# Performance work log

Hardware: AMD Instinct MI355X
Metric: run time of the kernel (lower is better)

Reference implementation:

```python
import jax, jax.numpy as jnp
import numpy as np

B, L, S, H, E, M = 16, 2048, 2048, 8, 64, 64  # batch, q len, kv len, heads, per-head dim, modes
SCALE = 1.0 / (512 * 512)  # 1/(in_channels*out_channels)


def setup_inputs() -> dict:
    key = jax.random.key(0)
    kq, kk, kv, kw1, kw2 = jax.random.split(key, 5)
    return {
        "q": jax.random.normal(kq, (B, L, H, E), dtype=jnp.float32),
        "k": jax.random.normal(kk, (B, S, H, E), dtype=jnp.float32),
        "v": jax.random.normal(kv, (B, S, H, E), dtype=jnp.float32),
        "weights_real": SCALE * jax.random.uniform(kw1, (H, E, E, M), dtype=jnp.float32),
        "weights_imag": SCALE * jax.random.uniform(kw2, (H, E, E, M), dtype=jnp.float32),
        "mask": jnp.zeros((1,), dtype=bool),  # unused by forward (kept for signature parity)
    }


def reference(q, k, v, weights_real, weights_imag, mask):
    # [B, L, H, E] -> [B, H, E, L]
    _q = jnp.transpose(q, (0, 2, 3, 1))
    _k = jnp.transpose(k, (0, 2, 3, 1))
    _v = jnp.transpose(v, (0, 2, 3, 1))

    # rFFT along time; mode_select_method='else' => index = range(M), a contiguous slice
    Qf = jnp.fft.rfft(_q, axis=-1)[..., :M]  # [B, H, E, M] complex
    Kf = jnp.fft.rfft(_k, axis=-1)[..., :M]
    Vf = jnp.fft.rfft(_v, axis=-1)[..., :M]

    # cross attention in frequency domain
    QK = jnp.einsum('bhex,bhey->bhxy', Qf, Kf)  # [B, H, M, M] complex
    QK = jnp.tanh(QK.real) + 1j * jnp.tanh(QK.imag)  # 'tanh' activation on re/im
    QKV = jnp.einsum('bhxy,bhey->bhex', QK, Vf)  # [B, H, E, M]

    W = (weights_real + 1j * weights_imag).astype(jnp.complex64)  # [H, E, O, M]
    QKVW = jnp.einsum('bhex,heox->bhox', QKV, W)  # [B, H, O, M]

    # scatter selected modes back into full half-spectrum, then inverse FFT
    Y = jnp.zeros((B, H, E, L // 2 + 1), dtype=jnp.complex64).at[..., :M].set(QKVW)
    y = jnp.fft.irfft(Y, n=L, axis=-1)  # [B, H, O, L] real
    return jnp.transpose(y, (0, 3, 1, 2))  # [B, L, H, O]
```

## Files before the change

### kernel.cpp

```cpp
#include <hip/hip_runtime.h>
#include <hip/hip_fp16.h>
#include <math.h>


#define NB 16
#define NL 2048
#define NH 8
#define NE 64
#define NM 64
#define NHE 512

typedef unsigned short ushort_t;
typedef __attribute__((ext_vector_type(8))) short short8;
typedef __attribute__((ext_vector_type(8))) _Float16 half8;
typedef __attribute__((ext_vector_type(4))) float f32x4;

__device__ inline void gld_lds16(const void* g, void* l) {
    __builtin_amdgcn_global_load_lds((const __attribute__((address_space(1))) unsigned int*)g,
                                     (__attribute__((address_space(3))) unsigned int*)l, 16, 0, 0);
}

__global__ __launch_bounds__(256) void k_tables_gemm(ushort_t* __restrict__ Twh,
                                                     ushort_t* __restrict__ Twl) {
    int i = blockIdx.x * 256 + threadIdx.x;
    int kj = i & 7;
    int l  = (i >> 3) & 63;
    int g  = (i >> 9) & 7;
    int ks = i >> 12;
    int mp = g * 16 + (l & 15);
    int kk = (l >> 4) * 8 + kj;
    int t = ks * 32 + kk;
    int m = mp >> 1;
    float ang = (float)((6.283185307179586476925287 / (double)NL) * (double)((m * t) & (NL - 1)));
    float val = (mp & 1) ? -sinf(ang) : cosf(ang);
    unsigned cb = __float_as_uint(val);
    ushort_t h = (ushort_t)(cb >> 16);
    float lo = val - __uint_as_float(cb & 0xffff0000u);
    unsigned lb = __float_as_uint(lo);
    unsigned r = lb + 0x7fffu + ((lb >> 16) & 1u);
    Twh[i] = h;
    Twl[i] = (ushort_t)(r >> 16);
}

__global__ __launch_bounds__(256) void k_tables_idft(ushort_t* __restrict__ Ih) {
    int i = blockIdx.x * 256 + threadIdx.x;
    int j = i & 7;
    int l = (i >> 3) & 63;
    int f = (i >> 9) & 15;
    int ks = (i >> 13) & 3;
    int tt = i >> 15;
    int t = tt * 256 + f * 16 + (l & 15);
    int kk = ks * 32 + (l >> 4) * 8 + j;
    int x = kk >> 1;
    float ang = (float)((6.283185307179586476925287 / (double)NL) * (double)((t * x) & (NL - 1)));
    float val = (kk & 1) ? -sinf(ang) : cosf(ang);
    Ih[i] = __half_as_ushort(__float2half(val));
}

__global__ __launch_bounds__(256, 3) void k_gemm(
    const float* __restrict__ q, const float* __restrict__ k, const float* __restrict__ v,
    const ushort_t* __restrict__ Twh, const ushort_t* __restrict__ Twl,
    float* __restrict__ Part) {
    const int bx = blockIdx.x & 7;
    const int kq = blockIdx.x >> 3;
    const int b  = blockIdx.y;
    const int z  = blockIdx.z;
    const float* __restrict__ in = (z == 0) ? q : ((z == 1) ? k : v);

    const int tid  = threadIdx.x;
    const int wid  = tid >> 6;
    const int lane = tid & 63;
    const int lr   = lane & 15;
    const int lg   = lane >> 4;
    const int wy   = wid >> 1;
    const int wx   = wid & 1;
    const int he0  = bx * 64;
    const int fx   = lg & 1;

    __shared__ float    As[2][32 * 64];
    __shared__ ushort_t Bh[2][4096];
    __shared__ ushort_t Bl[2][4096];

    f32x4 acc[2][4];
#pragma unroll
    for (int f = 0; f < 2; ++f)
#pragma unroll
        for (int j = 0; j < 4; ++j) acc[f][j] = (f32x4){0.f, 0.f, 0.f, 0.f};

    const size_t in_blk = ((size_t)b * NL + (size_t)kq * 1024) * NHE + he0;

#define STAGE(n, ksn)                                                                 \
    {                                                                                 \
        const ushort_t* gh = Twh + (size_t)(kq * 32 + (ksn)) * 4096;                  \
        const ushort_t* gl = Twl + (size_t)(kq * 32 + (ksn)) * 4096;                  \
        gld_lds16(gh + (size_t)tid * 8, &Bh[n][tid * 8]);                             \
        gld_lds16(gh + (size_t)(tid + 256) * 8, &Bh[n][(tid + 256) * 8]);             \
        gld_lds16(gl + (size_t)tid * 8, &Bl[n][tid * 8]);                             \
        gld_lds16(gl + (size_t)(tid + 256) * 8, &Bl[n][(tid + 256) * 8]);             \
        const float* ga = in + in_blk + (size_t)(ksn) * 32 * NHE;                     \
        _Pragma("unroll")                                                             \
        for (int p = 0; p < 2; ++p) {                                                 \
            int u = tid + p * 256;                                                    \
            int tloc = u >> 4, hc = u & 15;                                           \
            int hcs = hc ^ (((tloc >> 3) & 1) << 2);                                  \
            gld_lds16(ga + (size_t)tloc * NHE + hcs * 4, &As[n][u * 4]);              \
        }                                                                             \
    }

    STAGE(0, 0);

    int cur = 0;
    for (int ks = 0; ks < 32; ++ks) {
        __syncthreads();
        if (ks + 1 < 32) STAGE(cur ^ 1, ks + 1);

        const float* ac = &As[cur][0];
        const ushort_t* bhc = &Bh[cur][0];
        const ushort_t* blc = &Bl[cur][0];

        short8 bh8[4], bl8[4];
#pragma unroll
        for (int j = 0; j < 4; ++j) {
            bh8[j] = *(const short8*)&bhc[((wx * 4 + j) * 64 + lane) * 8];
            bl8[j] = *(const short8*)&blc[((wx * 4 + j) * 64 + lane) * 8];
        }

#pragma unroll
        for (int f = 0; f < 2; ++f) {
            const int col = wy * 32 + ((f ^ fx) << 4) + lr;
            float xa[8];
#pragma unroll
            for (int j = 0; j < 8; ++j) xa[j] = ac[(8 * lg + j) * 64 + col];
            union { unsigned u[4]; short8 s; } uh, ul;
#pragma unroll
            for (int p = 0; p < 4; ++p) {
                unsigned b0 = __float_as_uint(xa[2 * p]);
                unsigned b1 = __float_as_uint(xa[2 * p + 1]);
                uh.u[p] = (b0 >> 16) | (b1 & 0xffff0000u);
                float l0 = xa[2 * p]     - __uint_as_float(b0 & 0xffff0000u);
                float l1 = xa[2 * p + 1] - __uint_as_float(b1 & 0xffff0000u);
                unsigned lw;
                asm("v_cvt_pk_bf16_f32 %0, %1, %2" : "=v"(lw) : "v"(l0), "v"(l1));
                ul.u[p] = lw;
            }
#pragma unroll
            for (int j = 0; j < 4; ++j) {
                acc[f][j] = __builtin_amdgcn_mfma_f32_16x16x32_bf16(uh.s, bh8[j], acc[f][j], 0, 0, 0);
                acc[f][j] = __builtin_amdgcn_mfma_f32_16x16x32_bf16(ul.s, bh8[j], acc[f][j], 0, 0, 0);
                acc[f][j] = __builtin_amdgcn_mfma_f32_16x16x32_bf16(uh.s, bl8[j], acc[f][j], 0, 0, 0);
            }
        }
        cur ^= 1;
    }
#undef STAGE

    float* pout = Part + (size_t)(z * 2 + kq) * 1048576;
#pragma unroll
    for (int f = 0; f < 2; ++f) {
#pragma unroll
        for (int j = 0; j < 4; ++j) {
            const int col = wx * 64 + j * 16 + lr;
#pragma unroll
            for (int r = 0; r < 4; ++r) {
                const int he = he0 + wy * 32 + f * 16 + 4 * lg + r;
                pout[((size_t)b * NHE + he) * 128 + col] = acc[f][j][r];
            }
        }
    }
}

__global__ __launch_bounds__(256) void k_reduce(
    const float4* __restrict__ Part, float4* __restrict__ Qf,
    float4* __restrict__ Kf, float4* __restrict__ Vf) {
    int i = blockIdx.x * 256 + threadIdx.x;
    int z = i >> 18;
    int r = i & 262143;
    float4 a = Part[(size_t)(z * 2 + 0) * 262144 + r];
    float4 b = Part[(size_t)(z * 2 + 1) * 262144 + r];
    float4 s = make_float4(a.x + b.x, a.y + b.y, a.z + b.z, a.w + b.w);
    float4* o = (z == 0) ? Qf : ((z == 1) ? Kf : Vf);
    o[r] = s;
}

__global__ __launch_bounds__(256) void k_qk(
    const float2* __restrict__ Qf, const float2* __restrict__ Kf,
    float2* __restrict__ QKt) {
    const int bh = blockIdx.x;
    const int xh = blockIdx.y;
    const int tid = threadIdx.x;
    __shared__ float2 Qs[64 * 34];
    __shared__ float2 Ks[64 * 66];

    const float2* Qbase = Qf + (size_t)bh * (NE * NM);
    const float2* Kbase = Kf + (size_t)bh * (NE * NM);
#pragma unroll
    for (int j = 0; j < 4; ++j) {
        int n = tid + j * 256;
        int e = n >> 4, c = n & 15;
        float4 val = ((const float4*)(Qbase + e * NM + xh * 32))[c];
        *((float4*)&Qs[e * 34 + c * 2]) = val;
    }
#pragma unroll
    for (int j = 0; j < 8; ++j) {
        int n = tid + j * 256;
        int e = n >> 5, c = n & 31;
        float4 val = ((const float4*)(Kbase + e * NM))[c];
        *((float4*)&Ks[e * 66 + c * 2]) = val;
    }
    __syncthreads();

    const int yq = tid & 31, xq = tid >> 5;
    float accr[4][2], acci[4][2];
#pragma unroll
    for (int i = 0; i < 4; ++i)
#pragma unroll
        for (int j = 0; j < 2; ++j) { accr[i][j] = 0.f; acci[i][j] = 0.f; }

    for (int e = 0; e < 64; ++e) {
        float4 qa = *((float4*)&Qs[e * 34 + xq * 4]);
        float4 qb = *((float4*)&Qs[e * 34 + xq * 4 + 2]);
        float4 kk = *((float4*)&Ks[e * 66 + yq * 2]);
        float qr[4] = {qa.x, qa.z, qb.x, qb.z};
        float qi[4] = {qa.y, qa.w, qb.y, qb.w};
        float kr[2] = {kk.x, kk.z};
        float ki[2] = {kk.y, kk.w};
#pragma unroll
        for (int i = 0; i < 4; ++i) {
#pragma unroll
            for (int j = 0; j < 2; ++j) {
                accr[i][j] += qr[i] * kr[j] - qi[i] * ki[j];
                acci[i][j] += qr[i] * ki[j] + qi[i] * kr[j];
            }
        }
    }
    const int x0 = xh * 32 + xq * 4;
#pragma unroll
    for (int i = 0; i < 4; ++i) {
        float4 sv = make_float4(tanhf(accr[i][0]), tanhf(acci[i][0]),
                                tanhf(accr[i][1]), tanhf(acci[i][1]));
        *((float4*)&QKt[(size_t)bh * 4096 + (x0 + i) * 64 + yq * 2]) = sv;
    }
}

__global__ __launch_bounds__(256) void k_qkv(
    const float2* __restrict__ Vf, const float2* __restrict__ QKt,
    float2* __restrict__ QKV) {
    const int bh = blockIdx.x;
    const int eh = blockIdx.y;
    const int tid = threadIdx.x;
    __shared__ float2 Vs[32 * 66];
    __shared__ float2 Ps[64 * 66];

    const float2* Vbase = Vf + (size_t)bh * (NE * NM) + eh * 32 * NM;
    const float2* Pbase = QKt + (size_t)bh * 4096;
#pragma unroll
    for (int j = 0; j < 4; ++j) {
        int n = tid + j * 256;
        int r = n >> 5, c = n & 31;
        float4 val = ((const float4*)(Vbase + r * NM))[c];
        *((float4*)&Vs[r * 66 + c * 2]) = val;
    }
#pragma unroll
    for (int j = 0; j < 8; ++j) {
        int n = tid + j * 256;
        int r = n >> 5, c = n & 31;
        float4 val = ((const float4*)(Pbase + r * NM))[c];
        *((float4*)&Ps[r * 66 + c * 2]) = val;
    }
    __syncthreads();

    const int xq = tid & 15, eq2 = tid >> 4;
    const int x0 = xq * 4, e0 = eq2 * 2;
    float accr[2][4], acci[2][4];
#pragma unroll
    for (int i = 0; i < 2; ++i)
#pragma unroll
        for (int j = 0; j < 4; ++j) { accr[i][j] = 0.f; acci[i][j] = 0.f; }

    for (int yy = 0; yy < 64; ++yy) {
        float2 v0 = Vs[(e0 + 0) * 66 + yy];
        float2 v1 = Vs[(e0 + 1) * 66 + yy];
        float2 p0 = Ps[(x0 + 0) * 66 + yy];
        float2 p1 = Ps[(x0 + 1) * 66 + yy];
        float2 p2 = Ps[(x0 + 2) * 66 + yy];
        float2 p3 = Ps[(x0 + 3) * 66 + yy];
        float pr[4] = {p0.x, p1.x, p2.x, p3.x};
        float pi[4] = {p0.y, p1.y, p2.y, p3.y};
#pragma unroll
        for (int j = 0; j < 4; ++j) {
            accr[0][j] += v0.x * pr[j] - v0.y * pi[j];
            acci[0][j] += v0.x * pi[j] + v0.y * pr[j];
            accr[1][j] += v1.x * pr[j] - v1.y * pi[j];
            acci[1][j] += v1.x * pi[j] + v1.y * pr[j];
        }
    }
#pragma unroll
    for (int e = 0; e < 2; ++e) {
        float2* obase = QKV + (size_t)bh * 4096 + (eh * 32 + e0 + e) * 64 + x0;
        float4 s0 = make_float4(accr[e][0], acci[e][0], accr[e][1], acci[e][1]);
        float4 s1 = make_float4(accr[e][2], acci[e][2], accr[e][3], acci[e][3]);
        ((float4*)obase)[0] = s0;
        ((float4*)obase)[1] = s1;
    }
}

__global__ __launch_bounds__(256) void k_wt(
    const float* __restrict__ wr, const float* __restrict__ wi,
    float2* __restrict__ Wt) {
    const int e = blockIdx.x, h = blockIdx.y;
    const int tid = threadIdx.x;
    __shared__ float lr[64 * 68];
    __shared__ float li[64 * 68];
    const float* rbase = wr + (size_t)(h * NE + e) * NE * NM;
    const float* ibase = wi + (size_t)(h * NE + e) * NE * NM;
#pragma unroll
    for (int j = 0; j < 4; ++j) {
        int n = tid + j * 256;
        int o = n >> 4, x4 = n & 15;
        float4 r4 = ((const float4*)(rbase + o * NM))[x4];
        float4 i4 = ((const float4*)(ibase + o * NM))[x4];
        *((float4*)&lr[o * 68 + x4 * 4]) = r4;
        *((float4*)&li[o * 68 + x4 * 4]) = i4;
    }
    __syncthreads();
#pragma unroll
    for (int j = 0; j < 16; ++j) {
        int n = tid + j * 256;
        int x = n >> 6, o = n & 63;
        Wt[((size_t)(h * NM + x) * NE + e) * NE + o] =
            make_float2(lr[o * 68 + x], li[o * 68 + x]);
    }
}

__global__ __launch_bounds__(256) void k_qkvw(
    const float2* __restrict__ QKV, const float2* __restrict__ Wt,
    float2* __restrict__ QKVWs) {
    const int x = blockIdx.x, h = blockIdx.y;
    const int tid = threadIdx.x;
    const int o = tid & 63, bq = tid >> 6;
    float accr[4], acci[4];
#pragma unroll
    for (int j = 0; j < 4; ++j) { accr[j] = 0.f; acci[j] = 0.f; }

    const float2* wbase = Wt + (size_t)(h * NM + x) * NE * NE + o;
    for (int e = 0; e < 64; ++e) {
        float2 w = wbase[(size_t)e * NE];
#pragma unroll
        for (int j = 0; j < 4; ++j) {
            int b = bq * 4 + j;
            float2 a = QKV[((size_t)(b * NH + h) * NE + e) * NM + x];
            accr[j] += a.x * w.x - a.y * w.y;
            acci[j] += a.x * w.y + a.y * w.x;
        }
    }
    const float sc = (x == 0) ? 0.5f : 1.0f;
#pragma unroll
    for (int j = 0; j < 4; ++j) {
        int b = bq * 4 + j;
        QKVWs[((size_t)(b * NH + h) * NM + x) * NE + o] =
            make_float2(accr[j] * sc, acci[j] * sc);
    }
}

__global__ __launch_bounds__(256, 3) void k_idft(
    const float2* __restrict__ QKVWs, const ushort_t* __restrict__ Ih,
    float* __restrict__ yout) {
    const int tt = blockIdx.x;
    const int bh = blockIdx.y;
    const int b = bh >> 3, h = bh & 7;
    const int tid = threadIdx.x;
    const int wid = tid >> 6;
    const int lane = tid & 63;
    const int lr = lane & 15;
    const int lg = lane >> 4;

    __shared__ ushort_t Ta[8192];
    __shared__ unsigned Xs[4096];

    const float2* xb = QKVWs + (size_t)bh * 4096;
#pragma unroll
    for (int r = 0; r < 16; ++r) {
        int i = tid + r * 256;
        int x = i >> 6, o = i & 63;
        float2 val = xb[i];
        int ks = x >> 4;
        int lane2 = (((x & 15) >> 2) << 4) | (o & 15);
        int jn = o >> 4;
        unsigned pk = (unsigned)__half_as_ushort(__float2half(val.x)) |
                      ((unsigned)__half_as_ushort(__float2half(val.y)) << 16);
        Xs[((ks * 4 + jn) * 64 + lane2) * 4 + (x & 3)] = pk;
    }
    {
        const ushort_t* gh = Ih + (size_t)(tt * 4) * 8192;
#pragma unroll
        for (int p = 0; p < 4; ++p)
            gld_lds16(gh + (size_t)(tid + p * 256) * 8, &Ta[(tid + p * 256) * 8]);
    }
    __syncthreads();

    f32x4 acc[4][4];
#pragma unroll
    for (int m = 0; m < 4; ++m)
#pragma unroll
        for (int n = 0; n < 4; ++n) acc[m][n] = (f32x4){0.f, 0.f, 0.f, 0.f};

    const ushort_t* XsS = (const ushort_t*)Xs;
    for (int ks = 0; ks < 4; ++ks) {
        half8 ah[4], bx_[4];
#pragma unroll
        for (int m = 0; m < 4; ++m)
            ah[m] = *(const half8*)&Ta[((wid * 4 + m) * 64 + lane) * 8];
#pragma unroll
        for (int n = 0; n < 4; ++n)
            bx_[n] = *(const half8*)&XsS[((ks * 4 + n) * 64 + lane) * 8];
#pragma unroll
        for (int m = 0; m < 4; ++m)
#pragma unroll
            for (int n = 0; n < 4; ++n)
                acc[m][n] = __builtin_amdgcn_mfma_f32_16x16x32_f16(ah[m], bx_[n], acc[m][n], 0, 0, 0);
        if (ks < 3) {
            __syncthreads();
            const ushort_t* gh = Ih + (size_t)(tt * 4 + ks + 1) * 8192;
#pragma unroll
            for (int p = 0; p < 4; ++p)
                gld_lds16(gh + (size_t)(tid + p * 256) * 8, &Ta[(tid + p * 256) * 8]);
            __syncthreads();
        }
    }

    const int t0 = tt * 256 + wid * 64;
    const float inv = 1.f / 1024.f;
#pragma unroll
    for (int m = 0; m < 4; ++m) {
#pragma unroll
        for (int n = 0; n < 4; ++n) {
            const int o = n * 16 + lr;
#pragma unroll
            for (int r = 0; r < 4; ++r) {
                const int t = t0 + m * 16 + lg * 4 + r;
                yout[(((size_t)b * NL + t) * NH + h) * NE + o] = acc[m][n][r] * inv;
            }
        }
    }
}

extern "C" void kernel_launch(void* const* d_in, const int* in_sizes, int n_in,
                              void* d_out, int out_size, void* d_ws, size_t ws_size,
                              hipStream_t stream) {
    const float* q  = (const float*)d_in[0];
    const float* k  = (const float*)d_in[1];
    const float* v  = (const float*)d_in[2];
    const float* wr = (const float*)d_in[3];
    const float* wi = (const float*)d_in[4];
    float* out = (float*)d_out;

    char* w = (char*)d_ws;
    ushort_t* Twh  = (ushort_t*)w;
    ushort_t* Twl  = (ushort_t*)(w + 524288);
    ushort_t* Ih   = (ushort_t*)(w + 1048576);
    float2*   Qf   = (float2*)(w + 2097152);
    float2*   Kf   = (float2*)(w + 6291456);
    float2*   Vf   = (float2*)(w + 10485760);
    float*    Part = (float*)(w + 14680064);
    float2*   QKt  = (float2*)(w + 14680064);
    float2*   QKV  = (float2*)(w + 18874368);
    float2*   Wt   = (float2*)(w + 23068672);
    float2*   QKVWs= (float2*)(w + 39845888);

    hipLaunchKernelGGL(k_tables_gemm, dim3(1024), dim3(256), 0, stream, Twh, Twl);
    hipLaunchKernelGGL(k_tables_idft, dim3(1024), dim3(256), 0, stream, Ih);
    hipLaunchKernelGGL(k_gemm, dim3(16, 16, 3), dim3(256), 0, stream,
                       q, k, v, Twh, Twl, Part);
    hipLaunchKernelGGL(k_reduce, dim3(3072), dim3(256), 0, stream,
                       (const float4*)Part, (float4*)Qf, (float4*)Kf, (float4*)Vf);
    hipLaunchKernelGGL(k_qk, dim3(128, 2), dim3(256), 0, stream, Qf, Kf, QKt);
    hipLaunchKernelGGL(k_qkv, dim3(128, 2), dim3(256), 0, stream, Vf, QKt, QKV);
    hipLaunchKernelGGL(k_wt, dim3(64, 8), dim3(256), 0, stream, wr, wi, Wt);
    hipLaunchKernelGGL(k_qkvw, dim3(64, 8), dim3(256), 0, stream, QKV, Wt, QKVWs);
    hipLaunchKernelGGL(k_idft, dim3(8, 128), dim3(256), 0, stream, QKVWs, Ih, out);
}
```

Before: 155.3 us.

## Widen DFT GEMM tile to 128 channels and load A directly into registers

The forward-DFT GEMM kernel now has each block cover 128 head-channels instead of 64, with each wave owning 32 rows and all 128 frequency columns. The grid halves, so each twiddle tile staged in LDS is reused by twice as many rows. The fp32 input tile no longer goes through LDS; it is read straight from global memory into registers, double-buffered across an unrolled pair of k-steps, before the bf16 hi/lo split. This removes LDS traffic and LDS reads for A, but raises register pressure from 64 accumulator registers plus the prefetch buffers. It also gives fewer blocks (384) to fill the GPU and uses uncoalesced per-lane strided global loads.

```diff
diff --git a/kernel.cpp b/kernel.cpp
--- a/kernel.cpp
+++ b/kernel.cpp
@@ -61,8 +61,8 @@
     const float* __restrict__ q, const float* __restrict__ k, const float* __restrict__ v,
     const ushort_t* __restrict__ Twh, const ushort_t* __restrict__ Twl,
     float* __restrict__ Part) {
-    const int bx = blockIdx.x & 7;
-    const int kq = blockIdx.x >> 3;
+    const int bx = blockIdx.x & 3;
+    const int kq = blockIdx.x >> 2;
     const int b  = blockIdx.y;
     const int z  = blockIdx.z;
     const float* __restrict__ in = (z == 0) ? q : ((z == 1) ? k : v);
@@ -72,24 +72,21 @@
     const int lane = tid & 63;
     const int lr   = lane & 15;
     const int lg   = lane >> 4;
-    const int wy   = wid >> 1;
-    const int wx   = wid & 1;
-    const int he0  = bx * 64;
-    const int fx   = lg & 1;
-
-    __shared__ float    As[2][32 * 64];
+
     __shared__ ushort_t Bh[2][4096];
     __shared__ ushort_t Bl[2][4096];
 
-    f32x4 acc[2][4];
+    f32x4 acc[2][8];
 #pragma unroll
     for (int f = 0; f < 2; ++f)
 #pragma unroll
-        for (int j = 0; j < 4; ++j) acc[f][j] = (f32x4){0.f, 0.f, 0.f, 0.f};
-
-    const size_t in_blk = ((size_t)b * NL + (size_t)kq * 1024) * NHE + he0;
-
-#define STAGE(n, ksn)                                                                 \
+        for (int g = 0; g < 8; ++g) acc[f][g] = (f32x4){0.f, 0.f, 0.f, 0.f};
+
+    const float* pA = in + ((size_t)b * NL + (size_t)kq * 1024) * NHE + bx * 128 + wid * 32 + lr;
+
+    float arE[2][8], arO[2][8];
+
+#define STAGE_B(n, ksn)                                                               \
     {                                                                                 \
         const ushort_t* gh = Twh + (size_t)(kq * 32 + (ksn)) * 4096;                  \
         const ushort_t* gl = Twl + (size_t)(kq * 32 + (ksn)) * 4096;                  \
@@ -97,73 +94,81 @@
         gld_lds16(gh + (size_t)(tid + 256) * 8, &Bh[n][(tid + 256) * 8]);             \
         gld_lds16(gl + (size_t)tid * 8, &Bl[n][tid * 8]);                             \
         gld_lds16(gl + (size_t)(tid + 256) * 8, &Bl[n][(tid + 256) * 8]);             \
-        const float* ga = in + in_blk + (size_t)(ksn) * 32 * NHE;                     \
+    }
+
+#define LOADA(ar, ksn)                                                                \
+    {                                                                                 \
         _Pragma("unroll")                                                             \
-        for (int p = 0; p < 2; ++p) {                                                 \
-            int u = tid + p * 256;                                                    \
-            int tloc = u >> 4, hc = u & 15;                                           \
-            int hcs = hc ^ (((tloc >> 3) & 1) << 2);                                  \
-            gld_lds16(ga + (size_t)tloc * NHE + hcs * 4, &As[n][u * 4]);              \
+        for (int f = 0; f < 2; ++f) {                                                 \
+            _Pragma("unroll")                                                         \
+            for (int j = 0; j < 8; ++j)                                               \
+                ar[f][j] = pA[(size_t)((ksn) * 32 + lg * 8 + j) * NHE + f * 16];      \
         }                                                                             \
     }
 
-    STAGE(0, 0);
-
-    int cur = 0;
-    for (int ks = 0; ks < 32; ++ks) {
+#define COMPUTE(ar, n)                                                                \
+    {                                                                                 \
+        short8 ah[2], al[2];                                                          \
+        _Pragma("unroll")                                                             \
+        for (int f = 0; f < 2; ++f) {                                                 \
+            union { unsigned u[4]; short8 s; } uh, ul;                                \
+            _Pragma("unroll")                                                         \
+            for (int p = 0; p < 4; ++p) {                                             \
+                unsigned b0 = __float_as_uint(ar[f][2 * p]);                          \
+                unsigned b1 = __float_as_uint(ar[f][2 * p + 1]);                      \
+                uh.u[p] = (b0 >> 16) | (b1 & 0xffff0000u);                            \
+                float l0 = ar[f][2 * p]     - __uint_as_float(b0 & 0xffff0000u);      \
+                float l1 = ar[f][2 * p + 1] - __uint_as_float(b1 & 0xffff0000u);      \
+                unsigned lw;                                                          \
+                asm("v_cvt_pk_bf16_f32 %0, %1, %2" : "=v"(lw) : "v"(l0), "v"(l1));    \
+                ul.u[p] = lw;                                                         \
+            }                                                                         \
+            ah[f] = uh.s; al[f] = ul.s;                                               \
+        }                                                                             \
+        _Pragma("unroll")                                                             \
+        for (int g = 0; g < 8; ++g) {                                                 \
+            short8 bh8 = *(const short8*)&Bh[n][(g * 64 + lane) * 8];                 \
+            short8 bl8 = *(const short8*)&Bl[n][(g * 64 + lane) * 8];                 \
+            _Pragma("unroll")                                                         \
+            for (int f = 0; f < 2; ++f) {                                             \
+                acc[f][g] = __builtin_amdgcn_mfma_f32_16x16x32_bf16(ah[f], bh8, acc[f][g], 0, 0, 0); \
+                acc[f][g] = __builtin_amdgcn_mfma_f32_16x16x32_bf16(al[f], bh8, acc[f][g], 0, 0, 0); \
+                acc[f][g] = __builtin_amdgcn_mfma_f32_16x16x32_bf16(ah[f], bl8, acc[f][g], 0, 0, 0); \
+            }                                                                         \
+        }                                                                             \
+    }
+
+    STAGE_B(0, 0);
+    LOADA(arE, 0);
+
+#pragma unroll 1
+    for (int k2 = 0; k2 < 16; ++k2) {
+        const int ksB = 2 * k2 + 1;
         __syncthreads();
-        if (ks + 1 < 32) STAGE(cur ^ 1, ks + 1);
-
-        const float* ac = &As[cur][0];
-        const ushort_t* bhc = &Bh[cur][0];
-        const ushort_t* blc = &Bl[cur][0];
-
-        short8 bh8[4], bl8[4];
-#pragma unroll
-        for (int j = 0; j < 4; ++j) {
-            bh8[j] = *(const short8*)&bhc[((wx * 4 + j) * 64 + lane) * 8];
-            bl8[j] = *(const short8*)&blc[((wx * 4 + j) * 64 + lane) * 8];
-        }
-
-#pragma unroll
-        for (int f = 0; f < 2; ++f) {
-            const int col = wy * 32 + ((f ^ fx) << 4) + lr;
-            float xa[8];
-#pragma unroll
-            for (int j = 0; j < 8; ++j) xa[j] = ac[(8 * lg + j) * 64 + col];
-            union { unsigned u[4]; short8 s; } uh, ul;
-#pragma unroll
-            for (int p = 0; p < 4; ++p) {
-                unsigned b0 = __float_as_uint(xa[2 * p]);
-                unsigned b1 = __float_as_uint(xa[2 * p + 1]);
-                uh.u[p] = (b0 >> 16) | (b1 & 0xffff0000u);
-                float l0 = xa[2 * p]     - __uint_as_float(b0 & 0xffff0000u);
-                float l1 = xa[2 * p + 1] - __uint_as_float(b1 & 0xffff0000u);
-                unsigned lw;
-                asm("v_cvt_pk_bf16_f32 %0, %1, %2" : "=v"(lw) : "v"(l0), "v"(l1));
-                ul.u[p] = lw;
-            }
-#pragma unroll
-            for (int j = 0; j < 4; ++j) {
-                acc[f][j] = __builtin_amdgcn_mfma_f32_16x16x32_bf16(uh.s, bh8[j], acc[f][j], 0, 0, 0);
-                acc[f][j] = __builtin_amdgcn_mfma_f32_16x16x32_bf16(ul.s, bh8[j], acc[f][j], 0, 0, 0);
-                acc[f][j] = __builtin_amdgcn_mfma_f32_16x16x32_bf16(uh.s, bl8[j], acc[f][j], 0, 0, 0);
-            }
-        }
-        cur ^= 1;
-    }
-#undef STAGE
+        STAGE_B(1, ksB);
+        LOADA(arO, ksB);
+        COMPUTE(arE, 0);
+        __syncthreads();
+        if (k2 < 15) {
+            STAGE_B(0, ksB + 1);
+            LOADA(arE, ksB + 1);
+        }
+        COMPUTE(arO, 1);
+    }
+#undef STAGE_B
+#undef LOADA
+#undef COMPUTE
 
     float* pout = Part + (size_t)(z * 2 + kq) * 1048576;
 #pragma unroll
     for (int f = 0; f < 2; ++f) {
 #pragma unroll
-        for (int j = 0; j < 4; ++j) {
-            const int col = wx * 64 + j * 16 + lr;
+        for (int g = 0; g < 8; ++g) {
+            const int col = g * 16 + lr;
 #pragma unroll
             for (int r = 0; r < 4; ++r) {
-                const int he = he0 + wy * 32 + f * 16 + 4 * lg + r;
-                pout[((size_t)b * NHE + he) * 128 + col] = acc[f][j][r];
+                const int he = bx * 128 + wid * 32 + f * 16 + 4 * lg + r;
+                pout[((size_t)b * NHE + he) * 128 + col] = acc[f][g][r];
             }
         }
     }
@@ -469,7 +474,7 @@
 
     hipLaunchKernelGGL(k_tables_gemm, dim3(1024), dim3(256), 0, stream, Twh, Twl);
     hipLaunchKernelGGL(k_tables_idft, dim3(1024), dim3(256), 0, stream, Ih);
-    hipLaunchKernelGGL(k_gemm, dim3(16, 16, 3), dim3(256), 0, stream,
+    hipLaunchKernelGGL(k_gemm, dim3(8, 16, 3), dim3(256), 0, stream,
                        q, k, v, Twh, Twl, Part);
     hipLaunchKernelGGL(k_reduce, dim3(3072), dim3(256), 0, stream,
                        (const float4*)Part, (float4*)Qf, (float4*)Kf, (float4*)Vf);
```

Result: faster. 150.9 us (-2.8%).

## Fuse split-K reduction, QK tanh, and QKV into one kernel; merge table kernels

Applied to the files above, without the earlier changes.

Replaces the separate reduce, QK and QKV kernels with one kernel. It sums the two split-K partials directly while loading into LDS, computes tanh(QK) for half of the x modes, keeps it in shared memory, then loads V and produces QKV for that half. The two twiddle-table kernels are merged into one launch. This removes the intermediate Qf/Kf/Vf and QKt global round trips and cuts four launches, in exchange for each block redundantly re-reducing the K and V partials.

```diff
diff --git a/kernel.cpp b/kernel.cpp
--- a/kernel.cpp
+++ b/kernel.cpp
@@ -20,41 +20,43 @@
                                      (__attribute__((address_space(3))) unsigned int*)l, 16, 0, 0);
 }
 
-__global__ __launch_bounds__(256) void k_tables_gemm(ushort_t* __restrict__ Twh,
-                                                     ushort_t* __restrict__ Twl) {
-    int i = blockIdx.x * 256 + threadIdx.x;
-    int kj = i & 7;
-    int l  = (i >> 3) & 63;
-    int g  = (i >> 9) & 7;
-    int ks = i >> 12;
-    int mp = g * 16 + (l & 15);
-    int kk = (l >> 4) * 8 + kj;
-    int t = ks * 32 + kk;
-    int m = mp >> 1;
-    float ang = (float)((6.283185307179586476925287 / (double)NL) * (double)((m * t) & (NL - 1)));
-    float val = (mp & 1) ? -sinf(ang) : cosf(ang);
-    unsigned cb = __float_as_uint(val);
-    ushort_t h = (ushort_t)(cb >> 16);
-    float lo = val - __uint_as_float(cb & 0xffff0000u);
-    unsigned lb = __float_as_uint(lo);
-    unsigned r = lb + 0x7fffu + ((lb >> 16) & 1u);
-    Twh[i] = h;
-    Twl[i] = (ushort_t)(r >> 16);
-}
-
-__global__ __launch_bounds__(256) void k_tables_idft(ushort_t* __restrict__ Ih) {
-    int i = blockIdx.x * 256 + threadIdx.x;
-    int j = i & 7;
-    int l = (i >> 3) & 63;
-    int f = (i >> 9) & 15;
-    int ks = (i >> 13) & 3;
-    int tt = i >> 15;
-    int t = tt * 256 + f * 16 + (l & 15);
-    int kk = ks * 32 + (l >> 4) * 8 + j;
-    int x = kk >> 1;
-    float ang = (float)((6.283185307179586476925287 / (double)NL) * (double)((t * x) & (NL - 1)));
-    float val = (kk & 1) ? -sinf(ang) : cosf(ang);
-    Ih[i] = __half_as_ushort(__float2half(val));
+__global__ __launch_bounds__(256) void k_tables(ushort_t* __restrict__ Twh,
+                                                ushort_t* __restrict__ Twl,
+                                                ushort_t* __restrict__ Ih) {
+    const int blk = blockIdx.x;
+    if (blk < 1024) {
+        int i = blk * 256 + threadIdx.x;
+        int kj = i & 7;
+        int l  = (i >> 3) & 63;
+        int g  = (i >> 9) & 7;
+        int ks = i >> 12;
+        int mp = g * 16 + (l & 15);
+        int kk = (l >> 4) * 8 + kj;
+        int t = ks * 32 + kk;
+        int m = mp >> 1;
+        float ang = (float)((6.283185307179586476925287 / (double)NL) * (double)((m * t) & (NL - 1)));
+        float val = (mp & 1) ? -sinf(ang) : cosf(ang);
+        unsigned cb = __float_as_uint(val);
+        ushort_t h = (ushort_t)(cb >> 16);
+        float lo = val - __uint_as_float(cb & 0xffff0000u);
+        unsigned lb = __float_as_uint(lo);
+        unsigned r = lb + 0x7fffu + ((lb >> 16) & 1u);
+        Twh[i] = h;
+        Twl[i] = (ushort_t)(r >> 16);
+    } else {
+        int i = (blk - 1024) * 256 + threadIdx.x;
+        int j = i & 7;
+        int l = (i >> 3) & 63;
+        int f = (i >> 9) & 15;
+        int ks = (i >> 13) & 3;
+        int tt = i >> 15;
+        int t = tt * 256 + f * 16 + (l & 15);
+        int kk = ks * 32 + (l >> 4) * 8 + j;
+        int x = kk >> 1;
+        float ang = (float)((6.283185307179586476925287 / (double)NL) * (double)((t * x) & (NL - 1)));
+        float val = (kk & 1) ? -sinf(ang) : cosf(ang);
+        Ih[i] = __half_as_ushort(__float2half(val));
+    }
 }
 
 __global__ __launch_bounds__(256, 3) void k_gemm(
@@ -169,43 +171,40 @@
     }
 }
 
-__global__ __launch_bounds__(256) void k_reduce(
-    const float4* __restrict__ Part, float4* __restrict__ Qf,
-    float4* __restrict__ Kf, float4* __restrict__ Vf) {
-    int i = blockIdx.x * 256 + threadIdx.x;
-    int z = i >> 18;
-    int r = i & 262143;
-    float4 a = Part[(size_t)(z * 2 + 0) * 262144 + r];
-    float4 b = Part[(size_t)(z * 2 + 1) * 262144 + r];
-    float4 s = make_float4(a.x + b.x, a.y + b.y, a.z + b.z, a.w + b.w);
-    float4* o = (z == 0) ? Qf : ((z == 1) ? Kf : Vf);
-    o[r] = s;
-}
-
-__global__ __launch_bounds__(256) void k_qk(
-    const float2* __restrict__ Qf, const float2* __restrict__ Kf,
-    float2* __restrict__ QKt) {
+__global__ __launch_bounds__(256) void k_qkqkv(
+    const float* __restrict__ Part, float2* __restrict__ QKV) {
     const int bh = blockIdx.x;
     const int xh = blockIdx.y;
     const int tid = threadIdx.x;
-    __shared__ float2 Qs[64 * 34];
-    __shared__ float2 Ks[64 * 66];
-
-    const float2* Qbase = Qf + (size_t)bh * (NE * NM);
-    const float2* Kbase = Kf + (size_t)bh * (NE * NM);
+
+    __shared__ float2 bufA[64 * 34];
+    __shared__ float2 bufB[64 * 66];
+
+    const float4* P0 = (const float4*)Part;
+    const float4* P1 = P0 + 262144;
+    const float4* P2 = P0 + 2 * 262144;
+    const float4* P3 = P0 + 3 * 262144;
+    const float4* P4 = P0 + 4 * 262144;
+    const float4* P5 = P0 + 5 * 262144;
+    const size_t fb = (size_t)bh * 2048;
+
 #pragma unroll
     for (int j = 0; j < 4; ++j) {
         int n = tid + j * 256;
         int e = n >> 4, c = n & 15;
-        float4 val = ((const float4*)(Qbase + e * NM + xh * 32))[c];
-        *((float4*)&Qs[e * 34 + c * 2]) = val;
+        float4 a = P0[fb + e * 32 + xh * 16 + c];
+        float4 b = P1[fb + e * 32 + xh * 16 + c];
+        *((float4*)&bufA[e * 34 + c * 2]) =
+            make_float4(a.x + b.x, a.y + b.y, a.z + b.z, a.w + b.w);
     }
 #pragma unroll
     for (int j = 0; j < 8; ++j) {
         int n = tid + j * 256;
         int e = n >> 5, c = n & 31;
-        float4 val = ((const float4*)(Kbase + e * NM))[c];
-        *((float4*)&Ks[e * 66 + c * 2]) = val;
+        float4 a = P2[fb + e * 32 + c];
+        float4 b = P3[fb + e * 32 + c];
+        *((float4*)&bufB[e * 66 + c * 2]) =
+            make_float4(a.x + b.x, a.y + b.y, a.z + b.z, a.w + b.w);
     }
     __syncthreads();
 
@@ -217,9 +216,9 @@
         for (int j = 0; j < 2; ++j) { accr[i][j] = 0.f; acci[i][j] = 0.f; }
 
     for (int e = 0; e < 64; ++e) {
-        float4 qa = *((float4*)&Qs[e * 34 + xq * 4]);
-        float4 qb = *((float4*)&Qs[e * 34 + xq * 4 + 2]);
-        float4 kk = *((float4*)&Ks[e * 66 + yq * 2]);
+        float4 qa = *((float4*)&bufA[e * 34 + xq * 4]);
+        float4 qb = *((float4*)&bufA[e * 34 + xq * 4 + 2]);
+        float4 kk = *((float4*)&bufB[e * 66 + yq * 2]);
         float qr[4] = {qa.x, qa.z, qb.x, qb.z};
         float qi[4] = {qa.y, qa.w, qb.y, qb.w};
         float kr[2] = {kk.x, kk.z};
@@ -233,72 +232,57 @@
             }
         }
     }
-    const int x0 = xh * 32 + xq * 4;
+    __syncthreads();
+
+    float2* Ps = bufA;
+    const int x0 = xq * 4;
 #pragma unroll
     for (int i = 0; i < 4; ++i) {
         float4 sv = make_float4(tanhf(accr[i][0]), tanhf(acci[i][0]),
                                 tanhf(accr[i][1]), tanhf(acci[i][1]));
-        *((float4*)&QKt[(size_t)bh * 4096 + (x0 + i) * 64 + yq * 2]) = sv;
-    }
-}
-
-__global__ __launch_bounds__(256) void k_qkv(
-    const float2* __restrict__ Vf, const float2* __restrict__ QKt,
-    float2* __restrict__ QKV) {
-    const int bh = blockIdx.x;
-    const int eh = blockIdx.y;
-    const int tid = threadIdx.x;
-    __shared__ float2 Vs[32 * 66];
-    __shared__ float2 Ps[64 * 66];
-
-    const float2* Vbase = Vf + (size_t)bh * (NE * NM) + eh * 32 * NM;
-    const float2* Pbase = QKt + (size_t)bh * 4096;
-#pragma unroll
-    for (int j = 0; j < 4; ++j) {
-        int n = tid + j * 256;
-        int r = n >> 5, c = n & 31;
-        float4 val = ((const float4*)(Vbase + r * NM))[c];
-        *((float4*)&Vs[r * 66 + c * 2]) = val;
+        *((float4*)&Ps[(x0 + i) * 66 + yq * 2]) = sv;
     }
 #pragma unroll
     for (int j = 0; j < 8; ++j) {
         int n = tid + j * 256;
-        int r = n >> 5, c = n & 31;
-        float4 val = ((const float4*)(Pbase + r * NM))[c];
-        *((float4*)&Ps[r * 66 + c * 2]) = val;
+        int e = n >> 5, c = n & 31;
+        float4 a = P4[fb + e * 32 + c];
+        float4 b = P5[fb + e * 32 + c];
+        *((float4*)&bufB[e * 66 + c * 2]) =
+            make_float4(a.x + b.x, a.y + b.y, a.z + b.z, a.w + b.w);
     }
     __syncthreads();
 
-    const int xq = tid & 15, eq2 = tid >> 4;
-    const int x0 = xq * 4, e0 = eq2 * 2;
-    float accr[2][4], acci[2][4];
+    const int xq2 = tid & 7, eq2 = tid >> 3;
+    const int x2 = xq2 * 4, e0 = eq2 * 2;
+    float br[2][4], bi[2][4];
 #pragma unroll
     for (int i = 0; i < 2; ++i)
 #pragma unroll
-        for (int j = 0; j < 4; ++j) { accr[i][j] = 0.f; acci[i][j] = 0.f; }
+        for (int j = 0; j < 4; ++j) { br[i][j] = 0.f; bi[i][j] = 0.f; }
 
     for (int yy = 0; yy < 64; ++yy) {
-        float2 v0 = Vs[(e0 + 0) * 66 + yy];
-        float2 v1 = Vs[(e0 + 1) * 66 + yy];
-        float2 p0 = Ps[(x0 + 0) * 66 + yy];
-        float2 p1 = Ps[(x0 + 1) * 66 + yy];
-        float2 p2 = Ps[(x0 + 2) * 66 + yy];
-        float2 p3 = Ps[(x0 + 3) * 66 + yy];
+        float2 v0 = bufB[(e0 + 0) * 66 + yy];
+        float2 v1 = bufB[(e0 + 1) * 66 + yy];
+        float2 p0 = Ps[(x2 + 0) * 66 + yy];
+        float2 p1 = Ps[(x2 + 1) * 66 + yy];
+        float2 p2 = Ps[(x2 + 2) * 66 + yy];
+        float2 p3 = Ps[(x2 + 3) * 66 + yy];
         float pr[4] = {p0.x, p1.x, p2.x, p3.x};
         float pi[4] = {p0.y, p1.y, p2.y, p3.y};
 #pragma unroll
         for (int j = 0; j < 4; ++j) {
-            accr[0][j] += v0.x * pr[j] - v0.y * pi[j];
-            acci[0][j] += v0.x * pi[j] + v0.y * pr[j];
-            accr[1][j] += v1.x * pr[j] - v1.y * pi[j];
-            acci[1][j] += v1.x * pi[j] + v1.y * pr[j];
+            br[0][j] += v0.x * pr[j] - v0.y * pi[j];
+            bi[0][j] += v0.x * pi[j] + v0.y * pr[j];
+            br[1][j] += v1.x * pr[j] - v1.y * pi[j];
+            bi[1][j] += v1.x * pi[j] + v1.y * pr[j];
         }
     }
 #pragma unroll
     for (int e = 0; e < 2; ++e) {
-        float2* obase = QKV + (size_t)bh * 4096 + (eh * 32 + e0 + e) * 64 + x0;
-        float4 s0 = make_float4(accr[e][0], acci[e][0], accr[e][1], acci[e][1]);
-        float4 s1 = make_float4(accr[e][2], acci[e][2], accr[e][3], acci[e][3]);
+        float2* obase = QKV + (size_t)bh * 4096 + (e0 + e) * 64 + xh * 32 + x2;
+        float4 s0 = make_float4(br[e][0], bi[e][0], br[e][1], bi[e][1]);
+        float4 s1 = make_float4(br[e][2], bi[e][2], br[e][3], bi[e][3]);
         ((float4*)obase)[0] = s0;
         ((float4*)obase)[1] = s1;
     }
@@ -458,23 +442,15 @@
     ushort_t* Twh  = (ushort_t*)w;
     ushort_t* Twl  = (ushort_t*)(w + 524288);
     ushort_t* Ih   = (ushort_t*)(w + 1048576);
-    float2*   Qf   = (float2*)(w + 2097152);
-    float2*   Kf   = (float2*)(w + 6291456);
-    float2*   Vf   = (float2*)(w + 10485760);
+    float2*   QKV  = (float2*)(w + 2097152);
     float*    Part = (float*)(w + 14680064);
-    float2*   QKt  = (float2*)(w + 14680064);
-    float2*   QKV  = (float2*)(w + 18874368);
     float2*   Wt   = (float2*)(w + 23068672);
     float2*   QKVWs= (float2*)(w + 39845888);
 
-    hipLaunchKernelGGL(k_tables_gemm, dim3(1024), dim3(256), 0, stream, Twh, Twl);
-    hipLaunchKernelGGL(k_tables_idft, dim3(1024), dim3(256), 0, stream, Ih);
+    hipLaunchKernelGGL(k_tables, dim3(2048), dim3(256), 0, stream, Twh, Twl, Ih);
     hipLaunchKernelGGL(k_gemm, dim3(16, 16, 3), dim3(256), 0, stream,
                        q, k, v, Twh, Twl, Part);
-    hipLaunchKernelGGL(k_reduce, dim3(3072), dim3(256), 0, stream,
-                       (const float4*)Part, (float4*)Qf, (float4*)Kf, (float4*)Vf);
-    hipLaunchKernelGGL(k_qk, dim3(128, 2), dim3(256), 0, stream, Qf, Kf, QKt);
-    hipLaunchKernelGGL(k_qkv, dim3(128, 2), dim3(256), 0, stream, Vf, QKt, QKV);
+    hipLaunchKernelGGL(k_qkqkv, dim3(128, 2), dim3(256), 0, stream, Part, QKV);
     hipLaunchKernelGGL(k_wt, dim3(64, 8), dim3(256), 0, stream, wr, wi, Wt);
     hipLaunchKernelGGL(k_qkvw, dim3(64, 8), dim3(256), 0, stream, QKV, Wt, QKVWs);
     hipLaunchKernelGGL(k_idft, dim3(8, 128), dim3(256), 0, stream, QKVWs, Ih, out);
```

Result: faster. 149.2 us (-3.9%).
